# Kernel tuning notes

Hardware: AMD Instinct MI355X
Metric: run time of the kernel (lower is better)

The kernel has to match this reference:

```python
import jax, jax.numpy as jnp
import numpy as np


def setup_inputs() -> dict:
    key = jax.random.key(0)
    k1, k2, k3 = jax.random.split(key, 3)
    T, B, C, H, W = 8, 4, 128, 96, 96
    h = w = 384  # original visibility-map resolution
    values = jax.random.normal(k1, (T + 1, B, C, H, W), jnp.float32)
    tvmap = jax.random.uniform(k2, (B, 1, h, w), jnp.float32)
    rvmaps = jax.random.uniform(k3, (T, B, 1, h, w), jnp.float32)
    return {"values": values, "tvmap": tvmap, "rvmaps": rvmaps}


def _resize_bin(m, H, W):
    # bilinear resize (half-pixel centers == torch align_corners=False), then > 0.5 threshold
    r = jax.image.resize(m, m.shape[:-2] + (H, W), method="bilinear")
    return (r > 0.5).astype(m.dtype)


def reference(values, tvmap, rvmaps):
    t_feat = values[0]          # [B,C,H,W]
    r_feats = values[1:]        # [T,B,C,H,W]
    T, B, C, H, W = r_feats.shape

    tv = _resize_bin(tvmap, H, W)                           # [B,1,H,W]
    rv = jax.vmap(lambda m: _resize_bin(m, H, W))(rvmaps)   # [T,B,1,H,W]
    vmap_ = tv[None] * rv                                   # [T,B,1,H,W]

    # per-frame masked similarity score gs
    gs = jnp.sum(vmap_ * t_feat[None] * r_feats, axis=(-1, -2, -3))  # [T,B]
    v_sum = jnp.sum(vmap_[:, :, 0], axis=(-1, -2))                   # [T,B]
    empty = v_sum < 1e-4
    gs = jnp.where(empty, 0.0, gs) / (v_sum + empty.astype(gs.dtype)) / C

    gss = gs.transpose(1, 0)[:, None, :, None, None]   # [B,1,T,1,1]
    vmaps = rv.transpose(1, 2, 0, 3, 4)                # [B,1,T,H,W]

    # masked softmax over frame axis (dim=2) with zero-guard
    mv = gss * vmaps
    mx = jnp.max(mv, axis=2, keepdims=True)
    me = jnp.exp(mv - mx) * vmaps
    ms = jnp.sum(me, axis=2, keepdims=True)
    ms = ms + (ms < 1e-4).astype(ms.dtype)
    c_match = jax.lax.stop_gradient(me / ms)           # [B,1,T,H,W]

    rf = r_feats.transpose(1, 2, 0, 3, 4)              # [B,C,T,H,W]
    c_out = jnp.sum(rf * c_match, axis=2)              # [B,C,H,W]

    c_mask = jnp.sum(c_match * vmaps, axis=2)          # [B,1,H,W]
    c_mask = jax.lax.stop_gradient(1.0 - jnp.mean(c_mask, axis=1, keepdims=True))

    out = jnp.concatenate([t_feat, c_out, c_mask], axis=1)  # [B, 2C+1, H, W]
    return out, c_mask, gs
```

## Files before the change

kernel.cpp:

```cpp
#include <hip/hip_runtime.h>
#include <math.h>

#define T_ 8
#define B_ 4
#define C_ 128
#define HW_ 9216
#define IN_HW_ 147456

typedef float nat_f4 __attribute__((ext_vector_type(4)));

__device__ __forceinline__ double resize_px(const float* __restrict__ img, int y, int x) {
  static const double wm[8]  = {0.03125, 0.09375, 0.15625, 0.21875,
                                0.21875, 0.15625, 0.09375, 0.03125};
  static const double w0[8]  = {0.0, 0.0, 0.625/3.5, 0.875/3.5,
                                0.875/3.5, 0.625/3.5, 0.375/3.5, 0.125/3.5};
  static const double w95[8] = {0.125/3.5, 0.375/3.5, 0.625/3.5, 0.875/3.5,
                                0.875/3.5, 0.625/3.5, 0.0, 0.0};
  const double* wy = (y == 0) ? w0 : (y == 95 ? w95 : wm);
  const double* wx = (x == 0) ? w0 : (x == 95 ? w95 : wm);
  double acc = 0.0;
#pragma unroll
  for (int ky = 0; ky < 8; ++ky) {
    double wyv = wy[ky];
    if (wyv == 0.0) continue;
    int jy = 4 * y - 2 + ky;
    const float* row = img + jy * 384;
    double ra = 0.0;
#pragma unroll
    for (int kx = 0; kx < 8; ++kx) {
      double wxv = wx[kx];
      if (wxv == 0.0) continue;
      int jx = 4 * x - 2 + kx;
      ra += wxv * (double)row[jx];
    }
    acc += wyv * ra;
  }
  return acc;
}

__device__ __forceinline__ float block_sum_256(float v) {
  v += __shfl_xor(v, 1);
  v += __shfl_xor(v, 2);
  v += __shfl_xor(v, 4);
  v += __shfl_xor(v, 8);
  v += __shfl_xor(v, 16);
  v += __shfl_xor(v, 32);
  __shared__ float s[4];
  int lane = threadIdx.x & 63, wv = threadIdx.x >> 6;
  if (lane == 0) s[wv] = v;
  __syncthreads();
  return s[0] + s[1] + s[2] + s[3];
}

__global__ void k_init(float* __restrict__ v_sum) {
  if (threadIdx.x < T_ * B_) v_sum[threadIdx.x] = 0.f;
}

__global__ __launch_bounds__(256) void k_rv(const float* __restrict__ rvmaps,
                                            const float* __restrict__ tvmap,
                                            float* __restrict__ rv, float* __restrict__ vm,
                                            float* __restrict__ v_sum) {
  int tb = blockIdx.y;
  int b = tb % B_;
  int p = blockIdx.x * 256 + threadIdx.x;
  int y = p / 96, x = p % 96;
  float rvv = (resize_px(rvmaps + (size_t)tb * IN_HW_, y, x) > 0.5) ? 1.0f : 0.0f;
  float tvv = (resize_px(tvmap  + (size_t)b  * IN_HW_, y, x) > 0.5) ? 1.0f : 0.0f;
  float vmv = rvv * tvv;
  rv[(size_t)tb * HW_ + p] = rvv;
  vm[(size_t)tb * HW_ + p] = vmv;
  float s = block_sum_256(vmv);
  if (threadIdx.x == 0) atomicAdd(&v_sum[tb], s);
}

__global__ __launch_bounds__(256) void k_gs(const float* __restrict__ values,
                                            const float* __restrict__ vm,
                                            float* __restrict__ gs_part) {
  int ptile = blockIdx.x;
  int c     = blockIdx.y;
  int b     = blockIdx.z;
  int p0 = ptile * 1024 + threadIdx.x * 4;
  const float4 a = *(const float4*)(values + ((size_t)b * C_ + c) * HW_ + p0);
  float acc[T_];
#pragma unroll
  for (int t = 0; t < T_; ++t) {
    const float4 m = *(const float4*)(vm + ((size_t)(t * B_ + b)) * HW_ + p0);
    const float4 r = *(const float4*)(values + ((size_t)((1 + t) * B_ + b) * C_ + c) * HW_ + p0);
    acc[t] = m.x * a.x * r.x + m.y * a.y * r.y + m.z * a.z * r.z + m.w * a.w * r.w;
  }
  __shared__ float sred[4][T_];
  int lane = threadIdx.x & 63, wv = threadIdx.x >> 6;
#pragma unroll
  for (int t = 0; t < T_; ++t) {
    float v = acc[t];
    v += __shfl_xor(v, 1);
    v += __shfl_xor(v, 2);
    v += __shfl_xor(v, 4);
    v += __shfl_xor(v, 8);
    v += __shfl_xor(v, 16);
    v += __shfl_xor(v, 32);
    if (lane == 0) sred[wv][t] = v;
  }
  __syncthreads();
  if (threadIdx.x < T_) {
    int t = threadIdx.x;
    float s = sred[0][t] + sred[1][t] + sred[2][t] + sred[3][t];
    gs_part[((size_t)(t * B_ + b) * C_ + c) * 9 + ptile] = s;
  }
}

__global__ __launch_bounds__(256) void k_gsfin(const float* __restrict__ gs_part,
                                               const float* __restrict__ v_sum,
                                               float* __restrict__ gs,
                                               float* __restrict__ out_gs) {
  __shared__ float sred[32][8];
  int tb = threadIdx.x >> 3, j = threadIdx.x & 7;
  const float4* p = (const float4*)(gs_part + (size_t)tb * (C_ * 9) + j * 144);
  float s = 0.f;
#pragma unroll
  for (int i = 0; i < 36; ++i) {
    float4 v = p[i];
    s += v.x + v.y + v.z + v.w;
  }
  sred[tb][j] = s;
  __syncthreads();
  if (threadIdx.x < 32) {
    int i = threadIdx.x;
    float t = 0.f;
#pragma unroll
    for (int k = 0; k < 8; ++k) t += sred[i][k];
    float vs = v_sum[i];
    bool empty = vs < 1e-4f;
    float g = (empty ? 0.f : t) / (vs + (empty ? 1.f : 0.f)) / (float)C_;
    gs[i] = g;
    out_gs[i] = g;
  }
}

__global__ __launch_bounds__(256) void k_cm(const float* __restrict__ rv,
                                            const float* __restrict__ gs,
                                            float* __restrict__ cm,
                                            float* __restrict__ out,
                                            float* __restrict__ out_cmask) {
  int b = blockIdx.y;
  int p = blockIdx.x * 256 + threadIdx.x;
  __shared__ float gsh[T_];
  if (threadIdx.x < T_) gsh[threadIdx.x] = gs[threadIdx.x * B_ + b];
  __syncthreads();
  float rvv[T_], mv[T_];
  float mx = -1e30f;
#pragma unroll
  for (int t = 0; t < T_; ++t) {
    rvv[t] = rv[((size_t)(t * B_ + b)) * HW_ + p];
    mv[t] = gsh[t] * rvv[t];
    mx = fmaxf(mx, mv[t]);
  }
  float e[T_], ms = 0.f;
#pragma unroll
  for (int t = 0; t < T_; ++t) {
    e[t] = expf(mv[t] - mx) * rvv[t];
    ms += e[t];
  }
  if (ms < 1e-4f) ms += 1.f;
  float inv = 1.f / ms, cs = 0.f;
#pragma unroll
  for (int t = 0; t < T_; ++t) {
    float w = e[t] * inv;
    cm[((size_t)(t * B_ + b)) * HW_ + p] = w;
    cs += w * rvv[t];
  }
  float cmv = 1.f - cs;
  size_t outb = (size_t)b * 257 * HW_;
  out[outb + (size_t)256 * HW_ + p] = cmv;
  out_cmask[(size_t)b * HW_ + p] = cmv;
}

__global__ __launch_bounds__(256) void k_epi(const float* __restrict__ values,
                                             const float* __restrict__ cm,
                                             float* __restrict__ out) {
  int ctile = blockIdx.x;
  int ptile = blockIdx.y;
  int b     = blockIdx.z;
  int p0 = ptile * 1024 + threadIdx.x * 4;

  float4 w[T_];
#pragma unroll
  for (int t = 0; t < T_; ++t)
    w[t] = *(const float4*)(cm + ((size_t)(t * B_ + b)) * HW_ + p0);

  size_t outb = (size_t)b * 257 * HW_;
#pragma unroll 1
  for (int cc = 0; cc < 4; ++cc) {
    int c = ctile * 4 + cc;
    const float4 tf = *(const float4*)(values + ((size_t)b * C_ + c) * HW_ + p0);
    nat_f4 tfn = {tf.x, tf.y, tf.z, tf.w};
    __builtin_nontemporal_store(tfn, (nat_f4*)(out + outb + (size_t)c * HW_ + p0));
    float4 acc = {0.f, 0.f, 0.f, 0.f};
#pragma unroll
    for (int t = 0; t < T_; ++t) {
      const float4 r = *(const float4*)(values +
          ((size_t)((1 + t) * B_ + b) * C_ + c) * HW_ + p0);
      acc.x += w[t].x * r.x;
      acc.y += w[t].y * r.y;
      acc.z += w[t].z * r.z;
      acc.w += w[t].w * r.w;
    }
    nat_f4 accn = {acc.x, acc.y, acc.z, acc.w};
    __builtin_nontemporal_store(accn, (nat_f4*)(out + outb + (size_t)(C_ + c) * HW_ + p0));
  }
}

extern "C" void kernel_launch(void* const* d_in, const int* in_sizes, int n_in,
                              void* d_out, int out_size, void* d_ws, size_t ws_size,
                              hipStream_t stream) {
  const float* values = (const float*)d_in[0];
  const float* tvmap  = (const float*)d_in[1];
  const float* rvmaps = (const float*)d_in[2];
  float* out = (float*)d_out;

  float* ws      = (float*)d_ws;
  float* rv      = ws;
  float* vm      = rv + (size_t)T_ * B_ * HW_;
  float* cmw     = vm;
  float* gs_part = vm + (size_t)T_ * B_ * HW_;
  float* v_sum   = gs_part + (size_t)T_ * B_ * C_ * 9;
  float* gsar    = v_sum + T_ * B_;

  float* out_cmask = out + (size_t)B_ * 257 * HW_;
  float* out_gs    = out_cmask + (size_t)B_ * HW_;

  hipLaunchKernelGGL(k_init,  dim3(1),                 dim3(64),  0, stream, v_sum);
  hipLaunchKernelGGL(k_rv,    dim3(HW_ / 256, T_ * B_), dim3(256), 0, stream, rvmaps, tvmap, rv, vm, v_sum);
  hipLaunchKernelGGL(k_gs,    dim3(9, C_, B_),         dim3(256), 0, stream, values, vm, gs_part);
  hipLaunchKernelGGL(k_gsfin, dim3(1),                 dim3(256), 0, stream, gs_part, v_sum, gsar, out_gs);
  hipLaunchKernelGGL(k_cm,    dim3(HW_ / 256, B_),     dim3(256), 0, stream, rv, gsar, cmw, out, out_cmask);
  hipLaunchKernelGGL(k_epi,   dim3(32, 9, B_),         dim3(256), 0, stream, values, cmw, out);
}
```

Baseline: 349.2 us.

## Fuse pipeline into one cooperative persistent kernel with grid syncs

```diff
diff --git a/kernel.cpp b/kernel.cpp
--- a/kernel.cpp
+++ b/kernel.cpp
@@ -1,4 +1,5 @@
 #include <hip/hip_runtime.h>
+#include <hip/hip_cooperative_groups.h>
 #include <math.h>
 
 #define T_ 8
@@ -49,165 +50,231 @@
   int lane = threadIdx.x & 63, wv = threadIdx.x >> 6;
   if (lane == 0) s[wv] = v;
   __syncthreads();
-  return s[0] + s[1] + s[2] + s[3];
-}
-
-__global__ void k_init(float* __restrict__ v_sum) {
-  if (threadIdx.x < T_ * B_) v_sum[threadIdx.x] = 0.f;
-}
-
-__global__ __launch_bounds__(256) void k_rv(const float* __restrict__ rvmaps,
+  float r = s[0] + s[1] + s[2] + s[3];
+  __syncthreads();
+  return r;
+}
+
+
+__device__ __forceinline__ void phaseA(int bid, int nb,
+                                       const float* __restrict__ rvmaps,
+                                       const float* __restrict__ tvmap,
+                                       float* __restrict__ rv,
+                                       float* __restrict__ vm) {
+  const int tid = threadIdx.x;
+  for (int job = bid; job < 1152; job += nb) {
+    int tb = job / 36;
+    int b  = tb % B_;
+    int p  = (job % 36) * 256 + tid;
+    int y = p / 96, x = p % 96;
+    float rvv = (resize_px(rvmaps + (size_t)tb * IN_HW_, y, x) > 0.5) ? 1.0f : 0.0f;
+    float tvv = (resize_px(tvmap  + (size_t)b  * IN_HW_, y, x) > 0.5) ? 1.0f : 0.0f;
+    rv[(size_t)tb * HW_ + p] = rvv;
+    vm[(size_t)tb * HW_ + p] = rvv * tvv;
+  }
+}
+
+__device__ __forceinline__ void phaseB(int bid, int nb,
+                                       const float* __restrict__ values,
+                                       const float* __restrict__ vm,
+                                       float* __restrict__ gs_part,
+                                       float* __restrict__ v_sum) {
+  const int tid = threadIdx.x;
+  __shared__ float sred[4][T_];
+  for (int job = bid; job < 4640; job += nb) {
+    if (job < 4608) {
+      int ptile = job % 9;
+      int c     = (job / 9) % C_;
+      int b     = job / (9 * C_);
+      int p0 = ptile * 1024 + tid * 4;
+      const float4 a = *(const float4*)(values + ((size_t)b * C_ + c) * HW_ + p0);
+      float acc[T_];
+#pragma unroll
+      for (int t = 0; t < T_; ++t) {
+        const float4 m = *(const float4*)(vm + ((size_t)(t * B_ + b)) * HW_ + p0);
+        const float4 r = *(const float4*)(values + ((size_t)((1 + t) * B_ + b) * C_ + c) * HW_ + p0);
+        acc[t] = m.x * a.x * r.x + m.y * a.y * r.y + m.z * a.z * r.z + m.w * a.w * r.w;
+      }
+      int lane = tid & 63, wv = tid >> 6;
+#pragma unroll
+      for (int t = 0; t < T_; ++t) {
+        float v = acc[t];
+        v += __shfl_xor(v, 1);
+        v += __shfl_xor(v, 2);
+        v += __shfl_xor(v, 4);
+        v += __shfl_xor(v, 8);
+        v += __shfl_xor(v, 16);
+        v += __shfl_xor(v, 32);
+        if (lane == 0) sred[wv][t] = v;
+      }
+      __syncthreads();
+      if (tid < T_) {
+        int t = tid;
+        float s = sred[0][t] + sred[1][t] + sred[2][t] + sred[3][t];
+        gs_part[(size_t)(t * B_ + b) * (C_ * 9) + c * 9 + ptile] = s;
+      }
+      __syncthreads();
+    } else {
+      int tb = job - 4608;
+      const float4* p = (const float4*)(vm + (size_t)tb * HW_);
+      float s = 0.f;
+      for (int i = tid; i < HW_ / 4; i += 256) {
+        float4 v = p[i];
+        s += v.x + v.y + v.z + v.w;
+      }
+      s = block_sum_256(s);
+      if (tid == 0) v_sum[tb] = s;
+    }
+  }
+}
+
+__device__ __forceinline__ void phaseC(int bid,
+                                       const float* __restrict__ gs_part,
+                                       const float* __restrict__ v_sum,
+                                       float* __restrict__ gsar,
+                                       float* __restrict__ out_gs) {
+  const int tid = threadIdx.x;
+  if (bid < T_ * B_) {
+    int tb = bid;
+    const float4* p = (const float4*)(gs_part + (size_t)tb * (C_ * 9));
+    float s = 0.f;
+    for (int i = tid; i < (C_ * 9) / 4; i += 256) {
+      float4 v = p[i];
+      s += v.x + v.y + v.z + v.w;
+    }
+    s = block_sum_256(s);
+    if (tid == 0) {
+      float vs = v_sum[tb];
+      bool empty = vs < 1e-4f;
+      float g = (empty ? 0.f : s) / (vs + (empty ? 1.f : 0.f)) / (float)C_;
+      gsar[tb] = g;
+      out_gs[tb] = g;
+    }
+  }
+}
+
+__device__ __forceinline__ void phaseE(int bid, int nb,
+                                       const float* __restrict__ values,
+                                       const float* __restrict__ rv,
+                                       const float* __restrict__ gsar,
+                                       float* __restrict__ out,
+                                       float* __restrict__ out_cmask) {
+  const int tid = threadIdx.x;
+  for (int job = bid; job < 1152; job += nb) {
+    int b     = job / 288;
+    int rem   = job % 288;
+    int ptile = rem / 32;
+    int ctile = rem % 32;
+
+    float gsv[T_];
+#pragma unroll
+    for (int t = 0; t < T_; ++t) gsv[t] = gsar[t * B_ + b];
+
+    int p0 = ptile * 1024 + tid * 4;
+    float4 rv4[T_];
+#pragma unroll
+    for (int t = 0; t < T_; ++t)
+      rv4[t] = *(const float4*)(rv + ((size_t)(t * B_ + b)) * HW_ + p0);
+
+    float cm[T_][4];
+    float cmask[4];
+#pragma unroll
+    for (int j = 0; j < 4; ++j) {
+      float mv[T_];
+      float mx = -1e30f;
+#pragma unroll
+      for (int t = 0; t < T_; ++t) {
+        float rvv = ((const float*)&rv4[t])[j];
+        mv[t] = gsv[t] * rvv;
+        mx = fmaxf(mx, mv[t]);
+      }
+      float e[T_];
+      float ms = 0.f;
+#pragma unroll
+      for (int t = 0; t < T_; ++t) {
+        float rvv = ((const float*)&rv4[t])[j];
+        e[t] = expf(mv[t] - mx) * rvv;
+        ms += e[t];
+      }
+      if (ms < 1e-4f) ms += 1.f;
+      float inv = 1.f / ms;
+      float cs = 0.f;
+#pragma unroll
+      for (int t = 0; t < T_; ++t) {
+        cm[t][j] = e[t] * inv;
+        cs += cm[t][j] * ((const float*)&rv4[t])[j];
+      }
+      cmask[j] = 1.f - cs;
+    }
+
+    size_t outb = (size_t)b * 257 * HW_;
+#pragma unroll 1
+    for (int cc = 0; cc < 4; ++cc) {
+      int c = ctile * 4 + cc;
+      const float4 tf = *(const float4*)(values + ((size_t)b * C_ + c) * HW_ + p0);
+      nat_f4 tfn = {tf.x, tf.y, tf.z, tf.w};
+      __builtin_nontemporal_store(tfn, (nat_f4*)(out + outb + (size_t)c * HW_ + p0));
+      float4 acc = {0.f, 0.f, 0.f, 0.f};
+#pragma unroll
+      for (int t = 0; t < T_; ++t) {
+        const float4 r = *(const float4*)(values +
+            ((size_t)((1 + t) * B_ + b) * C_ + c) * HW_ + p0);
+        acc.x += cm[t][0] * r.x;
+        acc.y += cm[t][1] * r.y;
+        acc.z += cm[t][2] * r.z;
+        acc.w += cm[t][3] * r.w;
+      }
+      nat_f4 accn = {acc.x, acc.y, acc.z, acc.w};
+      __builtin_nontemporal_store(accn, (nat_f4*)(out + outb + (size_t)(C_ + c) * HW_ + p0));
+    }
+    if (ctile == 0) {
+      nat_f4 cmv = {cmask[0], cmask[1], cmask[2], cmask[3]};
+      __builtin_nontemporal_store(cmv, (nat_f4*)(out + outb + (size_t)256 * HW_ + p0));
+      __builtin_nontemporal_store(cmv, (nat_f4*)(out_cmask + (size_t)b * HW_ + p0));
+    }
+  }
+}
+
+__global__ __launch_bounds__(256, 4) void k_fused(
+    const float* __restrict__ values, const float* __restrict__ tvmap,
+    const float* __restrict__ rvmaps, float* __restrict__ rv,
+    float* __restrict__ vm, float* __restrict__ gs_part,
+    float* __restrict__ v_sum, float* __restrict__ gsar,
+    float* __restrict__ out, float* __restrict__ out_cmask,
+    float* __restrict__ out_gs) {
+  cooperative_groups::grid_group grid = cooperative_groups::this_grid();
+  phaseA(blockIdx.x, gridDim.x, rvmaps, tvmap, rv, vm);
+  grid.sync();
+  phaseB(blockIdx.x, gridDim.x, values, vm, gs_part, v_sum);
+  grid.sync();
+  phaseC(blockIdx.x, gs_part, v_sum, gsar, out_gs);
+  grid.sync();
+  phaseE(blockIdx.x, gridDim.x, values, rv, gsar, out, out_cmask);
+}
+
+__global__ __launch_bounds__(256) void k_pA(const float* __restrict__ rvmaps,
                                             const float* __restrict__ tvmap,
-                                            float* __restrict__ rv, float* __restrict__ vm,
+                                            float* __restrict__ rv, float* __restrict__ vm) {
+  phaseA(blockIdx.x, gridDim.x, rvmaps, tvmap, rv, vm);
+}
+__global__ __launch_bounds__(256) void k_pB(const float* __restrict__ values,
+                                            const float* __restrict__ vm,
+                                            float* __restrict__ gs_part,
                                             float* __restrict__ v_sum) {
-  int tb = blockIdx.y;
-  int b = tb % B_;
-  int p = blockIdx.x * 256 + threadIdx.x;
-  int y = p / 96, x = p % 96;
-  float rvv = (resize_px(rvmaps + (size_t)tb * IN_HW_, y, x) > 0.5) ? 1.0f : 0.0f;
-  float tvv = (resize_px(tvmap  + (size_t)b  * IN_HW_, y, x) > 0.5) ? 1.0f : 0.0f;
-  float vmv = rvv * tvv;
-  rv[(size_t)tb * HW_ + p] = rvv;
-  vm[(size_t)tb * HW_ + p] = vmv;
-  float s = block_sum_256(vmv);
-  if (threadIdx.x == 0) atomicAdd(&v_sum[tb], s);
-}
-
-__global__ __launch_bounds__(256) void k_gs(const float* __restrict__ values,
-                                            const float* __restrict__ vm,
-                                            float* __restrict__ gs_part) {
-  int ptile = blockIdx.x;
-  int c     = blockIdx.y;
-  int b     = blockIdx.z;
-  int p0 = ptile * 1024 + threadIdx.x * 4;
-  const float4 a = *(const float4*)(values + ((size_t)b * C_ + c) * HW_ + p0);
-  float acc[T_];
-#pragma unroll
-  for (int t = 0; t < T_; ++t) {
-    const float4 m = *(const float4*)(vm + ((size_t)(t * B_ + b)) * HW_ + p0);
-    const float4 r = *(const float4*)(values + ((size_t)((1 + t) * B_ + b) * C_ + c) * HW_ + p0);
-    acc[t] = m.x * a.x * r.x + m.y * a.y * r.y + m.z * a.z * r.z + m.w * a.w * r.w;
-  }
-  __shared__ float sred[4][T_];
-  int lane = threadIdx.x & 63, wv = threadIdx.x >> 6;
-#pragma unroll
-  for (int t = 0; t < T_; ++t) {
-    float v = acc[t];
-    v += __shfl_xor(v, 1);
-    v += __shfl_xor(v, 2);
-    v += __shfl_xor(v, 4);
-    v += __shfl_xor(v, 8);
-    v += __shfl_xor(v, 16);
-    v += __shfl_xor(v, 32);
-    if (lane == 0) sred[wv][t] = v;
-  }
-  __syncthreads();
-  if (threadIdx.x < T_) {
-    int t = threadIdx.x;
-    float s = sred[0][t] + sred[1][t] + sred[2][t] + sred[3][t];
-    gs_part[((size_t)(t * B_ + b) * C_ + c) * 9 + ptile] = s;
-  }
-}
-
-__global__ __launch_bounds__(256) void k_gsfin(const float* __restrict__ gs_part,
-                                               const float* __restrict__ v_sum,
-                                               float* __restrict__ gs,
-                                               float* __restrict__ out_gs) {
-  __shared__ float sred[32][8];
-  int tb = threadIdx.x >> 3, j = threadIdx.x & 7;
-  const float4* p = (const float4*)(gs_part + (size_t)tb * (C_ * 9) + j * 144);
-  float s = 0.f;
-#pragma unroll
-  for (int i = 0; i < 36; ++i) {
-    float4 v = p[i];
-    s += v.x + v.y + v.z + v.w;
-  }
-  sred[tb][j] = s;
-  __syncthreads();
-  if (threadIdx.x < 32) {
-    int i = threadIdx.x;
-    float t = 0.f;
-#pragma unroll
-    for (int k = 0; k < 8; ++k) t += sred[i][k];
-    float vs = v_sum[i];
-    bool empty = vs < 1e-4f;
-    float g = (empty ? 0.f : t) / (vs + (empty ? 1.f : 0.f)) / (float)C_;
-    gs[i] = g;
-    out_gs[i] = g;
-  }
-}
-
-__global__ __launch_bounds__(256) void k_cm(const float* __restrict__ rv,
-                                            const float* __restrict__ gs,
-                                            float* __restrict__ cm,
+  phaseB(blockIdx.x, gridDim.x, values, vm, gs_part, v_sum);
+}
+__global__ __launch_bounds__(256) void k_pC(const float* __restrict__ gs_part,
+                                            const float* __restrict__ v_sum,
+                                            float* __restrict__ gsar,
+                                            float* __restrict__ out_gs) {
+  phaseC(blockIdx.x, gs_part, v_sum, gsar, out_gs);
+}
+__global__ __launch_bounds__(256) void k_pE(const float* __restrict__ values,
+                                            const float* __restrict__ rv,
+                                            const float* __restrict__ gsar,
                                             float* __restrict__ out,
                                             float* __restrict__ out_cmask) {
-  int b = blockIdx.y;
-  int p = blockIdx.x * 256 + threadIdx.x;
-  __shared__ float gsh[T_];
-  if (threadIdx.x < T_) gsh[threadIdx.x] = gs[threadIdx.x * B_ + b];
-  __syncthreads();
-  float rvv[T_], mv[T_];
-  float mx = -1e30f;
-#pragma unroll
-  for (int t = 0; t < T_; ++t) {
-    rvv[t] = rv[((size_t)(t * B_ + b)) * HW_ + p];
-    mv[t] = gsh[t] * rvv[t];
-    mx = fmaxf(mx, mv[t]);
-  }
-  float e[T_], ms = 0.f;
-#pragma unroll
-  for (int t = 0; t < T_; ++t) {
-    e[t] = expf(mv[t] - mx) * rvv[t];
-    ms += e[t];
-  }
-  if (ms < 1e-4f) ms += 1.f;
-  float inv = 1.f / ms, cs = 0.f;
-#pragma unroll
-  for (int t = 0; t < T_; ++t) {
-    float w = e[t] * inv;
-    cm[((size_t)(t * B_ + b)) * HW_ + p] = w;
-    cs += w * rvv[t];
-  }
-  float cmv = 1.f - cs;
-  size_t outb = (size_t)b * 257 * HW_;
-  out[outb + (size_t)256 * HW_ + p] = cmv;
-  out_cmask[(size_t)b * HW_ + p] = cmv;
-}
-
-__global__ __launch_bounds__(256) void k_epi(const float* __restrict__ values,
-                                             const float* __restrict__ cm,
-                                             float* __restrict__ out) {
-  int ctile = blockIdx.x;
-  int ptile = blockIdx.y;
-  int b     = blockIdx.z;
-  int p0 = ptile * 1024 + threadIdx.x * 4;
-
-  float4 w[T_];
-#pragma unroll
-  for (int t = 0; t < T_; ++t)
-    w[t] = *(const float4*)(cm + ((size_t)(t * B_ + b)) * HW_ + p0);
-
-  size_t outb = (size_t)b * 257 * HW_;
-#pragma unroll 1
-  for (int cc = 0; cc < 4; ++cc) {
-    int c = ctile * 4 + cc;
-    const float4 tf = *(const float4*)(values + ((size_t)b * C_ + c) * HW_ + p0);
-    nat_f4 tfn = {tf.x, tf.y, tf.z, tf.w};
-    __builtin_nontemporal_store(tfn, (nat_f4*)(out + outb + (size_t)c * HW_ + p0));
-    float4 acc = {0.f, 0.f, 0.f, 0.f};
-#pragma unroll
-    for (int t = 0; t < T_; ++t) {
-      const float4 r = *(const float4*)(values +
-          ((size_t)((1 + t) * B_ + b) * C_ + c) * HW_ + p0);
-      acc.x += w[t].x * r.x;
-      acc.y += w[t].y * r.y;
-      acc.z += w[t].z * r.z;
-      acc.w += w[t].w * r.w;
-    }
-    nat_f4 accn = {acc.x, acc.y, acc.z, acc.w};
-    __builtin_nontemporal_store(accn, (nat_f4*)(out + outb + (size_t)(C_ + c) * HW_ + p0));
-  }
+  phaseE(blockIdx.x, gridDim.x, values, rv, gsar, out, out_cmask);
 }
 
 extern "C" void kernel_launch(void* const* d_in, const int* in_sizes, int n_in,
@@ -221,7 +288,6 @@
   float* ws      = (float*)d_ws;
   float* rv      = ws;
   float* vm      = rv + (size_t)T_ * B_ * HW_;
-  float* cmw     = vm;
   float* gs_part = vm + (size_t)T_ * B_ * HW_;
   float* v_sum   = gs_part + (size_t)T_ * B_ * C_ * 9;
   float* gsar    = v_sum + T_ * B_;
@@ -229,10 +295,30 @@
   float* out_cmask = out + (size_t)B_ * 257 * HW_;
   float* out_gs    = out_cmask + (size_t)B_ * HW_;
 
-  hipLaunchKernelGGL(k_init,  dim3(1),                 dim3(64),  0, stream, v_sum);
-  hipLaunchKernelGGL(k_rv,    dim3(HW_ / 256, T_ * B_), dim3(256), 0, stream, rvmaps, tvmap, rv, vm, v_sum);
-  hipLaunchKernelGGL(k_gs,    dim3(9, C_, B_),         dim3(256), 0, stream, values, vm, gs_part);
-  hipLaunchKernelGGL(k_gsfin, dim3(1),                 dim3(256), 0, stream, gs_part, v_sum, gsar, out_gs);
-  hipLaunchKernelGGL(k_cm,    dim3(HW_ / 256, B_),     dim3(256), 0, stream, rv, gsar, cmw, out, out_cmask);
-  hipLaunchKernelGGL(k_epi,   dim3(32, 9, B_),         dim3(256), 0, stream, values, cmw, out);
-}
+  static int coop_grid = 0;
+  if (coop_grid == 0) {
+    int maxb = 0;
+    hipError_t qe = hipOccupancyMaxActiveBlocksPerMultiprocessor(&maxb, k_fused, 256, 0);
+    if (qe != hipSuccess || maxb < 1) coop_grid = -1;
+    else {
+      long g = (long)maxb * 256;
+      coop_grid = (int)(g > 1024 ? 1024 : g);
+    }
+  }
+
+  hipError_t e = hipErrorUnknown;
+  if (coop_grid > 0) {
+    void* args[] = {(void*)&values, (void*)&tvmap, (void*)&rvmaps,
+                    (void*)&rv, (void*)&vm, (void*)&gs_part, (void*)&v_sum,
+                    (void*)&gsar, (void*)&out, (void*)&out_cmask, (void*)&out_gs};
+    e = hipLaunchCooperativeKernel((const void*)k_fused, dim3(coop_grid),
+                                   dim3(256), args, 0, stream);
+    if (e != hipSuccess) coop_grid = -1;
+  }
+  if (e != hipSuccess) {
+    hipLaunchKernelGGL(k_pA, dim3(1152), dim3(256), 0, stream, rvmaps, tvmap, rv, vm);
+    hipLaunchKernelGGL(k_pB, dim3(4640), dim3(256), 0, stream, values, vm, gs_part, v_sum);
+    hipLaunchKernelGGL(k_pC, dim3(32),   dim3(256), 0, stream, gs_part, v_sum, gsar, out_gs);
+    hipLaunchKernelGGL(k_pE, dim3(1152), dim3(256), 0, stream, values, rv, gsar, out, out_cmask);
+  }
+}
```

Result: slower. 558.9 us (+60.1%).

## Restructure pipeline: separable row-reuse resize, fuse softmax into epilogue, drop atomics

Applied to the files above, without the earlier changes.

```diff
diff --git a/kernel.cpp b/kernel.cpp
--- a/kernel.cpp
+++ b/kernel.cpp
@@ -9,34 +9,12 @@
 
 typedef float nat_f4 __attribute__((ext_vector_type(4)));
 
-__device__ __forceinline__ double resize_px(const float* __restrict__ img, int y, int x) {
-  static const double wm[8]  = {0.03125, 0.09375, 0.15625, 0.21875,
-                                0.21875, 0.15625, 0.09375, 0.03125};
-  static const double w0[8]  = {0.0, 0.0, 0.625/3.5, 0.875/3.5,
-                                0.875/3.5, 0.625/3.5, 0.375/3.5, 0.125/3.5};
-  static const double w95[8] = {0.125/3.5, 0.375/3.5, 0.625/3.5, 0.875/3.5,
-                                0.875/3.5, 0.625/3.5, 0.0, 0.0};
-  const double* wy = (y == 0) ? w0 : (y == 95 ? w95 : wm);
-  const double* wx = (x == 0) ? w0 : (x == 95 ? w95 : wm);
-  double acc = 0.0;
-#pragma unroll
-  for (int ky = 0; ky < 8; ++ky) {
-    double wyv = wy[ky];
-    if (wyv == 0.0) continue;
-    int jy = 4 * y - 2 + ky;
-    const float* row = img + jy * 384;
-    double ra = 0.0;
-#pragma unroll
-    for (int kx = 0; kx < 8; ++kx) {
-      double wxv = wx[kx];
-      if (wxv == 0.0) continue;
-      int jx = 4 * x - 2 + kx;
-      ra += wxv * (double)row[jx];
-    }
-    acc += wyv * ra;
-  }
-  return acc;
-}
+__device__ static const double d_wm[8]  = {0.03125, 0.09375, 0.15625, 0.21875,
+                                           0.21875, 0.15625, 0.09375, 0.03125};
+__device__ static const double d_w0[8]  = {0.0, 0.0, 0.625/3.5, 0.875/3.5,
+                                           0.875/3.5, 0.625/3.5, 0.375/3.5, 0.125/3.5};
+__device__ static const double d_w95[8] = {0.125/3.5, 0.375/3.5, 0.625/3.5, 0.875/3.5,
+                                           0.875/3.5, 0.625/3.5, 0.0, 0.0};
 
 __device__ __forceinline__ float block_sum_256(float v) {
   v += __shfl_xor(v, 1);
@@ -49,47 +27,111 @@
   int lane = threadIdx.x & 63, wv = threadIdx.x >> 6;
   if (lane == 0) s[wv] = v;
   __syncthreads();
-  return s[0] + s[1] + s[2] + s[3];
-}
-
-__global__ void k_init(float* __restrict__ v_sum) {
-  if (threadIdx.x < T_ * B_) v_sum[threadIdx.x] = 0.f;
-}
-
-__global__ __launch_bounds__(256) void k_rv(const float* __restrict__ rvmaps,
-                                            const float* __restrict__ tvmap,
-                                            float* __restrict__ rv, float* __restrict__ vm,
-                                            float* __restrict__ v_sum) {
-  int tb = blockIdx.y;
-  int b = tb % B_;
-  int p = blockIdx.x * 256 + threadIdx.x;
-  int y = p / 96, x = p % 96;
-  float rvv = (resize_px(rvmaps + (size_t)tb * IN_HW_, y, x) > 0.5) ? 1.0f : 0.0f;
-  float tvv = (resize_px(tvmap  + (size_t)b  * IN_HW_, y, x) > 0.5) ? 1.0f : 0.0f;
-  float vmv = rvv * tvv;
-  rv[(size_t)tb * HW_ + p] = rvv;
-  vm[(size_t)tb * HW_ + p] = vmv;
-  float s = block_sum_256(vmv);
-  if (threadIdx.x == 0) atomicAdd(&v_sum[tb], s);
+  float r = s[0] + s[1] + s[2] + s[3];
+  __syncthreads();
+  return r;
+}
+
+__global__ __launch_bounds__(384) void k_resize(const float* __restrict__ rvmaps,
+                                                const float* __restrict__ tvmap,
+                                                float* __restrict__ rv,
+                                                float* __restrict__ tv) {
+  const int job = blockIdx.y;
+  const float* img = (job < 32) ? rvmaps + (size_t)job * IN_HW_
+                                : tvmap  + (size_t)(job - 32) * IN_HW_;
+  float* dst = (job < 32) ? rv + (size_t)job * HW_
+                          : tv + (size_t)(job - 32) * HW_;
+  const int x  = threadIdx.x % 96;
+  const int yg = threadIdx.x / 96;
+  const int y0 = blockIdx.x * 16 + yg * 4;
+
+  const double* wys[4];
+#pragma unroll
+  for (int i = 0; i < 4; ++i) {
+    int y = y0 + i;
+    wys[i] = (y == 0) ? d_w0 : (y == 95 ? d_w95 : d_wm);
+  }
+
+  double acc0 = 0.0, acc1 = 0.0, acc2 = 0.0, acc3 = 0.0;
+  const int base = 4 * y0 - 2;
+  const int jy_lo = base < 0 ? 0 : base;
+  const int jy_hi_raw = 4 * (y0 + 3) + 5;
+  const int jy_hi = jy_hi_raw > 383 ? 383 : jy_hi_raw;
+
+  for (int jy = jy_lo; jy <= jy_hi; ++jy) {
+    const float* row = img + (size_t)jy * 384;
+    double ra;
+    if (x == 0) {
+      const float4 q0 = *(const float4*)(row);
+      const float4 q1 = *(const float4*)(row + 4);
+      ra = d_w0[2] * (double)q0.x + d_w0[3] * (double)q0.y +
+           d_w0[4] * (double)q0.z + d_w0[5] * (double)q0.w +
+           d_w0[6] * (double)q1.x + d_w0[7] * (double)q1.y;
+    } else if (x == 95) {
+      const float4 q0 = *(const float4*)(row + 376);
+      const float4 q1 = *(const float4*)(row + 380);
+      ra = d_w95[0] * (double)q0.z + d_w95[1] * (double)q0.w +
+           d_w95[2] * (double)q1.x + d_w95[3] * (double)q1.y +
+           d_w95[4] * (double)q1.z + d_w95[5] * (double)q1.w;
+    } else {
+      const int b0 = 4 * x - 4;
+      const float4 q0 = *(const float4*)(row + b0);
+      const float4 q1 = *(const float4*)(row + b0 + 4);
+      const float4 q2 = *(const float4*)(row + b0 + 8);
+      ra = d_wm[0] * (double)q0.z + d_wm[1] * (double)q0.w +
+           d_wm[2] * (double)q1.x + d_wm[3] * (double)q1.y +
+           d_wm[4] * (double)q1.z + d_wm[5] * (double)q1.w +
+           d_wm[6] * (double)q2.x + d_wm[7] * (double)q2.y;
+    }
+    {
+      int ky = jy - base;
+      if (ky >= 0 && ky < 8) acc0 += wys[0][ky] * ra;
+      ky -= 4;
+      if (ky >= 0 && ky < 8) acc1 += wys[1][ky] * ra;
+      ky -= 4;
+      if (ky >= 0 && ky < 8) acc2 += wys[2][ky] * ra;
+      ky -= 4;
+      if (ky >= 0 && ky < 8) acc3 += wys[3][ky] * ra;
+    }
+  }
+  dst[(size_t)(y0 + 0) * 96 + x] = (acc0 > 0.5) ? 1.0f : 0.0f;
+  dst[(size_t)(y0 + 1) * 96 + x] = (acc1 > 0.5) ? 1.0f : 0.0f;
+  dst[(size_t)(y0 + 2) * 96 + x] = (acc2 > 0.5) ? 1.0f : 0.0f;
+  dst[(size_t)(y0 + 3) * 96 + x] = (acc3 > 0.5) ? 1.0f : 0.0f;
 }
 
 __global__ __launch_bounds__(256) void k_gs(const float* __restrict__ values,
-                                            const float* __restrict__ vm,
-                                            float* __restrict__ gs_part) {
-  int ptile = blockIdx.x;
-  int c     = blockIdx.y;
-  int b     = blockIdx.z;
-  int p0 = ptile * 1024 + threadIdx.x * 4;
-  const float4 a = *(const float4*)(values + ((size_t)b * C_ + c) * HW_ + p0);
+                                            const float* __restrict__ rv,
+                                            const float* __restrict__ tv,
+                                            float* __restrict__ gs_part,
+                                            float* __restrict__ out) {
+  const int ptile = blockIdx.x;
+  const int c     = blockIdx.y;
+  const int b     = blockIdx.z;
+  const int tid   = threadIdx.x;
+  const int p0 = ptile * 1024 + tid * 4;
+
+  const float4 a   = *(const float4*)(values + ((size_t)b * C_ + c) * HW_ + p0);
+  const float4 tvv = *(const float4*)(tv + (size_t)b * HW_ + p0);
+
+  {
+    nat_f4 an = {a.x, a.y, a.z, a.w};
+    __builtin_nontemporal_store(an,
+        (nat_f4*)(out + (size_t)b * 257 * HW_ + (size_t)c * HW_ + p0));
+  }
+
   float acc[T_];
 #pragma unroll
   for (int t = 0; t < T_; ++t) {
-    const float4 m = *(const float4*)(vm + ((size_t)(t * B_ + b)) * HW_ + p0);
+    const float4 rv4 = *(const float4*)(rv + ((size_t)(t * B_ + b)) * HW_ + p0);
     const float4 r = *(const float4*)(values + ((size_t)((1 + t) * B_ + b) * C_ + c) * HW_ + p0);
-    acc[t] = m.x * a.x * r.x + m.y * a.y * r.y + m.z * a.z * r.z + m.w * a.w * r.w;
-  }
+    const float mx_ = rv4.x * tvv.x, my_ = rv4.y * tvv.y;
+    const float mz_ = rv4.z * tvv.z, mw_ = rv4.w * tvv.w;
+    acc[t] = mx_ * a.x * r.x + my_ * a.y * r.y + mz_ * a.z * r.z + mw_ * a.w * r.w;
+  }
+
   __shared__ float sred[4][T_];
-  int lane = threadIdx.x & 63, wv = threadIdx.x >> 6;
+  const int lane = tid & 63, wv = tid >> 6;
 #pragma unroll
   for (int t = 0; t < T_; ++t) {
     float v = acc[t];
@@ -102,111 +144,119 @@
     if (lane == 0) sred[wv][t] = v;
   }
   __syncthreads();
-  if (threadIdx.x < T_) {
-    int t = threadIdx.x;
-    float s = sred[0][t] + sred[1][t] + sred[2][t] + sred[3][t];
-    gs_part[((size_t)(t * B_ + b) * C_ + c) * 9 + ptile] = s;
-  }
-}
-
-__global__ __launch_bounds__(256) void k_gsfin(const float* __restrict__ gs_part,
-                                               const float* __restrict__ v_sum,
-                                               float* __restrict__ gs,
-                                               float* __restrict__ out_gs) {
-  __shared__ float sred[32][8];
-  int tb = threadIdx.x >> 3, j = threadIdx.x & 7;
-  const float4* p = (const float4*)(gs_part + (size_t)tb * (C_ * 9) + j * 144);
+  if (tid < T_) {
+    const int t = tid;
+    const float s = sred[0][t] + sred[1][t] + sred[2][t] + sred[3][t];
+    gs_part[(size_t)(t * B_ + b) * (C_ * 9) + c * 9 + ptile] = s;
+  }
+}
+
+__global__ __launch_bounds__(256) void k_fin(const float* __restrict__ rv,
+                                             const float* __restrict__ tv,
+                                             const float* __restrict__ gs_part,
+                                             float* __restrict__ gsar,
+                                             float* __restrict__ out_gs) {
+  const int tb = blockIdx.x;
+  const int b  = tb % B_;
+  const int tid = threadIdx.x;
+
+  const float4* pr = (const float4*)(rv + (size_t)tb * HW_);
+  const float4* pt = (const float4*)(tv + (size_t)b  * HW_);
+  float vs = 0.f;
+  for (int i = tid; i < HW_ / 4; i += 256) {
+    const float4 r = pr[i], t = pt[i];
+    vs += r.x * t.x + r.y * t.y + r.z * t.z + r.w * t.w;
+  }
+  vs = block_sum_256(vs);
+
+  const float4* pg = (const float4*)(gs_part + (size_t)tb * (C_ * 9));
   float s = 0.f;
-#pragma unroll
-  for (int i = 0; i < 36; ++i) {
-    float4 v = p[i];
+  for (int i = tid; i < (C_ * 9) / 4; i += 256) {
+    const float4 v = pg[i];
     s += v.x + v.y + v.z + v.w;
   }
-  sred[tb][j] = s;
-  __syncthreads();
-  if (threadIdx.x < 32) {
-    int i = threadIdx.x;
-    float t = 0.f;
-#pragma unroll
-    for (int k = 0; k < 8; ++k) t += sred[i][k];
-    float vs = v_sum[i];
-    bool empty = vs < 1e-4f;
-    float g = (empty ? 0.f : t) / (vs + (empty ? 1.f : 0.f)) / (float)C_;
-    gs[i] = g;
-    out_gs[i] = g;
-  }
-}
-
-__global__ __launch_bounds__(256) void k_cm(const float* __restrict__ rv,
-                                            const float* __restrict__ gs,
-                                            float* __restrict__ cm,
-                                            float* __restrict__ out,
-                                            float* __restrict__ out_cmask) {
-  int b = blockIdx.y;
-  int p = blockIdx.x * 256 + threadIdx.x;
+  s = block_sum_256(s);
+
+  if (tid == 0) {
+    const bool empty = vs < 1e-4f;
+    const float g = (empty ? 0.f : s) / (vs + (empty ? 1.f : 0.f)) / (float)C_;
+    gsar[tb] = g;
+    out_gs[tb] = g;
+  }
+}
+
+__global__ __launch_bounds__(256) void k_epi(const float* __restrict__ values,
+                                             const float* __restrict__ rv,
+                                             const float* __restrict__ gs,
+                                             float* __restrict__ out,
+                                             float* __restrict__ out_cmask) {
+  const int ctile = blockIdx.x;
+  const int ptile = blockIdx.y;
+  const int b     = blockIdx.z;
+  const int tid   = threadIdx.x;
   __shared__ float gsh[T_];
-  if (threadIdx.x < T_) gsh[threadIdx.x] = gs[threadIdx.x * B_ + b];
-  __syncthreads();
-  float rvv[T_], mv[T_];
-  float mx = -1e30f;
-#pragma unroll
-  for (int t = 0; t < T_; ++t) {
-    rvv[t] = rv[((size_t)(t * B_ + b)) * HW_ + p];
-    mv[t] = gsh[t] * rvv[t];
-    mx = fmaxf(mx, mv[t]);
-  }
-  float e[T_], ms = 0.f;
-#pragma unroll
-  for (int t = 0; t < T_; ++t) {
-    e[t] = expf(mv[t] - mx) * rvv[t];
-    ms += e[t];
-  }
-  if (ms < 1e-4f) ms += 1.f;
-  float inv = 1.f / ms, cs = 0.f;
-#pragma unroll
-  for (int t = 0; t < T_; ++t) {
-    float w = e[t] * inv;
-    cm[((size_t)(t * B_ + b)) * HW_ + p] = w;
-    cs += w * rvv[t];
-  }
-  float cmv = 1.f - cs;
-  size_t outb = (size_t)b * 257 * HW_;
-  out[outb + (size_t)256 * HW_ + p] = cmv;
-  out_cmask[(size_t)b * HW_ + p] = cmv;
-}
-
-__global__ __launch_bounds__(256) void k_epi(const float* __restrict__ values,
-                                             const float* __restrict__ cm,
-                                             float* __restrict__ out) {
-  int ctile = blockIdx.x;
-  int ptile = blockIdx.y;
-  int b     = blockIdx.z;
-  int p0 = ptile * 1024 + threadIdx.x * 4;
-
-  float4 w[T_];
+  if (tid < T_) gsh[tid] = gs[tid * B_ + b];
+  __syncthreads();
+
+  const int p0 = ptile * 1024 + tid * 4;
+
+  float4 rv4[T_];
 #pragma unroll
   for (int t = 0; t < T_; ++t)
-    w[t] = *(const float4*)(cm + ((size_t)(t * B_ + b)) * HW_ + p0);
-
-  size_t outb = (size_t)b * 257 * HW_;
+    rv4[t] = *(const float4*)(rv + ((size_t)(t * B_ + b)) * HW_ + p0);
+
+  float cm[T_][4];
+  float cmask[4];
+#pragma unroll
+  for (int j = 0; j < 4; ++j) {
+    float mv[T_];
+    float mx = -1e30f;
+#pragma unroll
+    for (int t = 0; t < T_; ++t) {
+      const float rvv = ((const float*)&rv4[t])[j];
+      mv[t] = gsh[t] * rvv;
+      mx = fmaxf(mx, mv[t]);
+    }
+    float e[T_];
+    float ms = 0.f;
+#pragma unroll
+    for (int t = 0; t < T_; ++t) {
+      const float rvv = ((const float*)&rv4[t])[j];
+      e[t] = expf(mv[t] - mx) * rvv;
+      ms += e[t];
+    }
+    if (ms < 1e-4f) ms += 1.f;
+    const float inv = 1.f / ms;
+    float cs = 0.f;
+#pragma unroll
+    for (int t = 0; t < T_; ++t) {
+      cm[t][j] = e[t] * inv;
+      cs += cm[t][j] * ((const float*)&rv4[t])[j];
+    }
+    cmask[j] = 1.f - cs;
+  }
+
+  const size_t outb = (size_t)b * 257 * HW_;
 #pragma unroll 1
   for (int cc = 0; cc < 4; ++cc) {
-    int c = ctile * 4 + cc;
-    const float4 tf = *(const float4*)(values + ((size_t)b * C_ + c) * HW_ + p0);
-    nat_f4 tfn = {tf.x, tf.y, tf.z, tf.w};
-    __builtin_nontemporal_store(tfn, (nat_f4*)(out + outb + (size_t)c * HW_ + p0));
+    const int c = ctile * 4 + cc;
     float4 acc = {0.f, 0.f, 0.f, 0.f};
 #pragma unroll
     for (int t = 0; t < T_; ++t) {
       const float4 r = *(const float4*)(values +
           ((size_t)((1 + t) * B_ + b) * C_ + c) * HW_ + p0);
-      acc.x += w[t].x * r.x;
-      acc.y += w[t].y * r.y;
-      acc.z += w[t].z * r.z;
-      acc.w += w[t].w * r.w;
+      acc.x += cm[t][0] * r.x;
+      acc.y += cm[t][1] * r.y;
+      acc.z += cm[t][2] * r.z;
+      acc.w += cm[t][3] * r.w;
     }
     nat_f4 accn = {acc.x, acc.y, acc.z, acc.w};
     __builtin_nontemporal_store(accn, (nat_f4*)(out + outb + (size_t)(C_ + c) * HW_ + p0));
+  }
+  if (ctile == 0) {
+    nat_f4 cmv = {cmask[0], cmask[1], cmask[2], cmask[3]};
+    __builtin_nontemporal_store(cmv, (nat_f4*)(out + outb + (size_t)256 * HW_ + p0));
+    __builtin_nontemporal_store(cmv, (nat_f4*)(out_cmask + (size_t)b * HW_ + p0));
   }
 }
 
@@ -220,19 +270,15 @@
 
   float* ws      = (float*)d_ws;
   float* rv      = ws;
-  float* vm      = rv + (size_t)T_ * B_ * HW_;
-  float* cmw     = vm;
-  float* gs_part = vm + (size_t)T_ * B_ * HW_;
-  float* v_sum   = gs_part + (size_t)T_ * B_ * C_ * 9;
-  float* gsar    = v_sum + T_ * B_;
+  float* tv      = rv + (size_t)T_ * B_ * HW_;
+  float* gs_part = tv + (size_t)B_ * HW_;
+  float* gsar    = gs_part + (size_t)T_ * B_ * C_ * 9;
 
   float* out_cmask = out + (size_t)B_ * 257 * HW_;
   float* out_gs    = out_cmask + (size_t)B_ * HW_;
 
-  hipLaunchKernelGGL(k_init,  dim3(1),                 dim3(64),  0, stream, v_sum);
-  hipLaunchKernelGGL(k_rv,    dim3(HW_ / 256, T_ * B_), dim3(256), 0, stream, rvmaps, tvmap, rv, vm, v_sum);
-  hipLaunchKernelGGL(k_gs,    dim3(9, C_, B_),         dim3(256), 0, stream, values, vm, gs_part);
-  hipLaunchKernelGGL(k_gsfin, dim3(1),                 dim3(256), 0, stream, gs_part, v_sum, gsar, out_gs);
-  hipLaunchKernelGGL(k_cm,    dim3(HW_ / 256, B_),     dim3(256), 0, stream, rv, gsar, cmw, out, out_cmask);
-  hipLaunchKernelGGL(k_epi,   dim3(32, 9, B_),         dim3(256), 0, stream, values, cmw, out);
-}
+  hipLaunchKernelGGL(k_resize, dim3(6, 36),      dim3(384), 0, stream, rvmaps, tvmap, rv, tv);
+  hipLaunchKernelGGL(k_gs,     dim3(9, C_, B_),  dim3(256), 0, stream, values, rv, tv, gs_part, out);
+  hipLaunchKernelGGL(k_fin,    dim3(32),         dim3(256), 0, stream, rv, tv, gs_part, gsar, out_gs);
+  hipLaunchKernelGGL(k_epi,    dim3(32, 9, B_),  dim3(256), 0, stream, values, rv, gsar, out, out_cmask);
+}
```

New measurement: 322.1 us. -7.8%, faster.
